# Kernel optimization log

Measured on AMD Instinct MI355X. Metric: run time of the kernel, lower is better.

The kernel has to match this reference:

```python
import jax, jax.numpy as jnp
import numpy as np

MIN_NORM = 1e-15
EPS = 1e-5
C_CURV = 1.0  # args.c

def _norm(x):
    return jnp.clip(jnp.linalg.norm(x, axis=-1, keepdims=True), MIN_NORM)

def artanh(x):
    x = jnp.clip(x, -1.0 + EPS, 1.0 - EPS)
    return 0.5 * (jnp.log1p(x) - jnp.log1p(-x))

def proj(x, c):
    # clip points to stay strictly inside the Poincare ball
    norm = _norm(x)
    maxnorm = (1.0 - EPS) / jnp.sqrt(c)
    return jnp.where(norm > maxnorm, x / norm * maxnorm, x)

def expmap0(u, c):
    sqrt_c = jnp.sqrt(c)
    u_norm = _norm(u)
    return jnp.tanh(sqrt_c * u_norm) * u / (sqrt_c * u_norm)

def logmap0(p, c):
    sqrt_c = jnp.sqrt(c)
    p_norm = _norm(p)
    return artanh(sqrt_c * p_norm) * p / (sqrt_c * p_norm)

def mobius_add(x, y, c):
    x2 = jnp.sum(x * x, axis=-1, keepdims=True)
    y2 = jnp.sum(y * y, axis=-1, keepdims=True)
    xy = jnp.sum(x * y, axis=-1, keepdims=True)
    num = (1.0 + 2.0 * c * xy + c * y2) * x + (1.0 - c * x2) * y
    denom = 1.0 + 2.0 * c * xy + c * c * x2 * y2
    return num / jnp.clip(denom, MIN_NORM)

def mobius_matvec(W, x, c):
    sqrt_c = jnp.sqrt(c)
    x_norm = _norm(x)
    mx = x @ W.T
    mx_norm = _norm(mx)
    return jnp.tanh(mx_norm / x_norm * artanh(sqrt_c * x_norm)) * mx / (mx_norm * sqrt_c)

def poincare_dist(x, y, c):
    sqrt_c = jnp.sqrt(c)
    d = _norm(mobius_add(-x, y, c))[..., 0]
    return 2.0 / sqrt_c * artanh(sqrt_c * d)

def hgnn_layer(h, adj, W, b, c):
    # HypLinear: mobius matvec + hyperbolic bias
    mv = proj(mobius_matvec(W, h, c), c)
    hyp_b = proj(expmap0(b, c), c)
    h = proj(mobius_add(mv, hyp_b, c), c)
    # HypAgg: aggregate in tangent space at origin
    h = proj(expmap0(adj @ logmap0(h, c), c), c)
    # HypAct: relu in tangent space
    return proj(expmap0(jax.nn.relu(logmap0(h, c)), c), c)

def setup_inputs() -> dict:
    key = jax.random.key(0)
    ks = jax.random.split(key, 10)
    N, D, C, NC, NODE_C, L = 8192, 128, 64, 7, 7, 4
    x = jax.random.normal(ks[0], (N, D), jnp.float32)
    adj = jax.random.uniform(ks[1], (N, N), jnp.float32) / N  # row-stochastic-ish dense adjacency
    graph_indicator = jax.random.randint(ks[2], (N,), 0, 1)
    W_conv = jax.random.normal(ks[3], (L, D, D), jnp.float32) / np.sqrt(D)
    b_conv = jax.random.normal(ks[4], (L, D), jnp.float32) * 0.01
    centroids = jax.random.normal(ks[5], (C, D), jnp.float32) * 0.1
    W_mlp = jax.random.normal(ks[6], (NC, C), jnp.float32) * 0.1
    b_mlp = jnp.zeros((NC,), jnp.float32)
    W_mlp1 = jax.random.normal(ks[7], (NODE_C, D), jnp.float32) * 0.1
    b_mlp1 = jnp.zeros((NODE_C,), jnp.float32)
    return {"x": x, "adj": adj, "graph_indicator": graph_indicator,
            "W_conv": W_conv, "b_conv": b_conv, "centroids": centroids,
            "W_mlp": W_mlp, "b_mlp": b_mlp, "W_mlp1": W_mlp1, "b_mlp1": b_mlp1}

def reference(x, adj, graph_indicator, W_conv, b_conv, centroids, W_mlp, b_mlp, W_mlp1, b_mlp1):
    c = C_CURV
    # proj_tan0 is identity for PoincareBall
    h = proj(expmap0(x, c), c)
    # 2 residual blocks, each with 2 HGNN layers; shortcut is identity (in_dim == out_dim)
    for blk in range(2):
        res = h
        for j in range(2):
            idx = blk * 2 + j
            h = hgnn_layer(h, adj, W_conv[idx], b_conv[idx], c)
        h = h + res  # Euclidean residual, as in the source
    # CentroidDistance: pairwise hyperbolic distance [N, C]
    node_centroid_dist = poincare_dist(h[:, None, :], centroids[None, :, :], c)
    readout = jnp.mean(node_centroid_dist, axis=0, keepdims=True)  # [1, C]
    h_r = logmap0(readout, c)  # proj_tan0(logmap0(.)) -> identity proj_tan0
    logits = jax.nn.softmax(h_r @ W_mlp.T + b_mlp, axis=0)[None]        # [1,1,NC]
    h1 = logmap0(h, c)
    logits_node = jax.nn.softmax(h1 @ W_mlp1.T + b_mlp1, axis=0)[None]  # [1,N,node_classes]
    return (logits, logits_node, h_r)
```

## Files before the change

### kernel.cpp

```cpp
#include <hip/hip_runtime.h>

#define MIN_NORM 1e-15f
#define EPSV 1e-5f
#define MAXN (1.0f - EPSV)
#define NN 8192
#define DD 128

typedef unsigned short u16;
typedef __bf16 bf16x8 __attribute__((ext_vector_type(8)));
typedef float f32x4 __attribute__((ext_vector_type(4)));

__device__ __forceinline__ float wave_sum(float v) {
#pragma unroll
  for (int off = 32; off > 0; off >>= 1) v += __shfl_xor(v, off, 64);
  return v;
}

__device__ __forceinline__ float artanh_f(float x) {
  x = fminf(fmaxf(x, -1.0f + EPSV), 1.0f - EPSV);
  return 0.5f * (log1pf(x) - log1pf(-x));
}

__device__ __forceinline__ u16 f2bf(float f) {
  unsigned u = __float_as_uint(f);
  unsigned r = (u + 0x7fffu + ((u >> 16) & 1u)) >> 16;
  return (u16)r;
}
__device__ __forceinline__ float bf2f(u16 b) { return __uint_as_float(((unsigned)b) << 16); }

__device__ __forceinline__ unsigned fenc(float x) {
  unsigned u = __float_as_uint(x);
  return (u & 0x80000000u) ? ~u : (u | 0x80000000u);
}
__device__ __forceinline__ float fdec(unsigned k) {
  unsigned u = (k & 0x80000000u) ? (k & 0x7fffffffu) : ~k;
  return __uint_as_float(u);
}

__device__ __forceinline__ void gload16(const u16* g, u16* l) {
  __builtin_amdgcn_global_load_lds((const __attribute__((address_space(1))) void*)(g),
                                   (__attribute__((address_space(3))) void*)(l), 16, 0, 0);
}

__global__ __launch_bounds__(256) void gemm_adj(const u16* __restrict__ A,
                                                const u16* __restrict__ Bt,
                                                float* __restrict__ Cp,
                                                int KC) {
  __shared__ __align__(16) u16 Ash[3 * 64 * 64];
  __shared__ __align__(16) u16 Bsh[3 * 128 * 64];

  const int tid = threadIdx.x;
  const int lane = tid & 63;
  const int w = tid >> 6;
  const int wm = w >> 1, wn = w & 1;
  const int lrow = lane & 15;
  const int lq = lane >> 4;
  const int m0 = blockIdx.x * 64;
  const int kt0 = (blockIdx.y * KC) >> 6;
  const int bxK = blockIdx.x * (NN >> 6);

  f32x4 acc[2][4];
#pragma unroll
  for (int a = 0; a < 2; a++)
#pragma unroll
    for (int b = 0; b < 4; b++)
#pragma unroll
      for (int r = 0; r < 4; r++) acc[a][b][r] = 0.0f;

#define STAGE(bf, tkt)                                                          \
  do {                                                                          \
    const u16* at = A + (((size_t)(bxK + (tkt))) << 12) + (lane << 3);          \
    _Pragma("unroll") for (int ii = 0; ii < 2; ii++)                            \
      gload16(at + ((ii * 4 + w) << 9), &Ash[(bf) * 4096 + ((ii * 4 + w) << 9)]); \
    const u16* bt2 = Bt + (((size_t)(tkt)) << 13) + (lane << 3);                \
    _Pragma("unroll") for (int ii = 0; ii < 4; ii++)                            \
      gload16(bt2 + ((ii * 4 + w) << 9), &Bsh[(bf) * 8192 + ((ii * 4 + w) << 9)]); \
  } while (0)

#define COMPUTE(bf)                                                             \
  do {                                                                          \
    const int abase = (bf) * 4096, bbase = (bf) * 8192;                         \
    _Pragma("unroll") for (int ks = 0; ks < 2; ks++) {                          \
      const int lc = ks * 4 + lq;                                               \
      bf16x8 af[2], bfr[4];                                                     \
      _Pragma("unroll") for (int ti = 0; ti < 2; ti++) {                        \
        int r = wm * 32 + ti * 16 + lrow;                                       \
        af[ti] = *(const bf16x8*)&Ash[abase + r * 64 + ((lc ^ (r & 7)) << 3)];  \
      }                                                                         \
      _Pragma("unroll") for (int tj = 0; tj < 4; tj++) {                        \
        int n = wn * 64 + tj * 16 + lrow;                                       \
        bfr[tj] = *(const bf16x8*)&Bsh[bbase + n * 64 + ((lc ^ (n & 7)) << 3)]; \
      }                                                                         \
      _Pragma("unroll") for (int ti = 0; ti < 2; ti++)                          \
        _Pragma("unroll") for (int tj = 0; tj < 4; tj++)                        \
          acc[ti][tj] = __builtin_amdgcn_mfma_f32_16x16x32_bf16(af[ti], bfr[tj], acc[ti][tj], 0, 0, 0); \
    }                                                                           \
  } while (0)

  const int nt = KC >> 6;
  STAGE(0, kt0);
  STAGE(1, kt0 + 1);
  for (int t = 0; t < nt - 1; t++) {
    asm volatile("s_waitcnt vmcnt(6)" ::: "memory");
    __builtin_amdgcn_s_barrier();
    if (t + 2 < nt) STAGE((t + 2) % 3, kt0 + t + 2);
    COMPUTE(t % 3);
  }
  asm volatile("s_waitcnt vmcnt(0)" ::: "memory");
  __builtin_amdgcn_s_barrier();
  COMPUTE((nt - 1) % 3);
#undef STAGE
#undef COMPUTE

  float* C = Cp + (size_t)blockIdx.y * NN * 128;
#pragma unroll
  for (int ti = 0; ti < 2; ti++)
#pragma unroll
    for (int tj = 0; tj < 4; tj++)
#pragma unroll
      for (int r = 0; r < 4; r++) {
        int row = m0 + wm * 32 + ti * 16 + lq * 4 + r;
        int col = wn * 64 + tj * 16 + lrow;
        C[(size_t)row * 128 + col] = acc[ti][tj][r];
      }
}

__global__ __launch_bounds__(256) void wgemm_mid(const u16* __restrict__ A,
                                                 const u16* __restrict__ Bt,
                                                 const float* __restrict__ hnorm,
                                                 const float* __restrict__ eb,
                                                 const float* __restrict__ ey2,
                                                 u16* __restrict__ uT2) {
  __shared__ __align__(16) u16 Ash[3 * 64 * 64];
  __shared__ __align__(16) u16 Bsh[3 * 128 * 64];

  const int tid = threadIdx.x;
  const int lane = tid & 63;
  const int w = tid >> 6;
  const int wm = w >> 1, wn = w & 1;
  const int lrow = lane & 15;
  const int lq = lane >> 4;
  const int m0 = blockIdx.x * 64;
  const int srow = lane >> 3, spc = lane & 7;
  const int K = 384;
  const u16* Ap = A + (size_t)m0 * K;

  f32x4 acc[2][4];
#pragma unroll
  for (int a = 0; a < 2; a++)
#pragma unroll
    for (int b = 0; b < 4; b++)
#pragma unroll
      for (int r = 0; r < 4; r++) acc[a][b][r] = 0.0f;

#define STAGE(bf, kk)                                                           \
  do {                                                                          \
    _Pragma("unroll") for (int ii = 0; ii < 2; ii++) {                          \
      int rw = ((ii * 4 + w) << 3) + srow;                                      \
      gload16(Ap + (size_t)rw * K + (kk) + ((spc ^ (rw & 7)) << 3),             \
              &Ash[(bf) * 4096 + ((ii * 4 + w) << 9)]);                         \
    }                                                                           \
    _Pragma("unroll") for (int ii = 0; ii < 4; ii++) {                          \
      int rw = ((ii * 4 + w) << 3) + srow;                                      \
      gload16(Bt + (size_t)rw * K + (kk) + ((spc ^ (rw & 7)) << 3),             \
              &Bsh[(bf) * 8192 + ((ii * 4 + w) << 9)]);                         \
    }                                                                           \
  } while (0)

#define COMPUTE(bf)                                                             \
  do {                                                                          \
    const int abase = (bf) * 4096, bbase = (bf) * 8192;                         \
    _Pragma("unroll") for (int ks = 0; ks < 2; ks++) {                          \
      const int lc = ks * 4 + lq;                                               \
      bf16x8 af[2], bfr[4];                                                     \
      _Pragma("unroll") for (int ti = 0; ti < 2; ti++) {                        \
        int r = wm * 32 + ti * 16 + lrow;                                       \
        af[ti] = *(const bf16x8*)&Ash[abase + r * 64 + ((lc ^ (r & 7)) << 3)];  \
      }                                                                         \
      _Pragma("unroll") for (int tj = 0; tj < 4; tj++) {                        \
        int n = wn * 64 + tj * 16 + lrow;                                       \
        bfr[tj] = *(const bf16x8*)&Bsh[bbase + n * 64 + ((lc ^ (n & 7)) << 3)]; \
      }                                                                         \
      _Pragma("unroll") for (int ti = 0; ti < 2; ti++)                          \
        _Pragma("unroll") for (int tj = 0; tj < 4; tj++)                        \
          acc[ti][tj] = __builtin_amdgcn_mfma_f32_16x16x32_bf16(af[ti], bfr[tj], acc[ti][tj], 0, 0, 0); \
    }                                                                           \
  } while (0)

  const int nt = 6;
  STAGE(0, 0);
  STAGE(1, 64);
  for (int t = 0; t < nt - 1; t++) {
    asm volatile("s_waitcnt vmcnt(6)" ::: "memory");
    __builtin_amdgcn_s_barrier();
    if (t + 2 < nt) STAGE((t + 2) % 3, (t + 2) * 64);
    COMPUTE(t % 3);
  }
  asm volatile("s_waitcnt vmcnt(0)" ::: "memory");
  __builtin_amdgcn_s_barrier();
  COMPUTE((nt - 1) % 3);
#undef STAGE
#undef COMPUTE

  float ecol[4];
#pragma unroll
  for (int tj = 0; tj < 4; tj++) ecol[tj] = eb[wn * 64 + tj * 16 + lrow];

  float* sred = (float*)Ash;
#pragma unroll
  for (int ti = 0; ti < 2; ti++)
#pragma unroll
    for (int r = 0; r < 4; r++) {
      float p2 = 0.f, pe = 0.f;
#pragma unroll
      for (int tj = 0; tj < 4; tj++) {
        float v = acc[ti][tj][r];
        p2 = fmaf(v, v, p2);
        pe = fmaf(v, ecol[tj], pe);
      }
#pragma unroll
      for (int off = 1; off < 16; off <<= 1) {
        p2 += __shfl_xor(p2, off, 64);
        pe += __shfl_xor(pe, off, 64);
      }
      if (lrow == 0) {
        int row = wm * 32 + ti * 16 + lq * 4 + r;
        sred[row * 4 + wn * 2 + 0] = p2;
        sred[row * 4 + wn * 2 + 1] = pe;
      }
    }
  __syncthreads();

  const float y2v = *ey2;
  u16* tb = uT2 + ((size_t)blockIdx.x << 13);
#pragma unroll
  for (int ti = 0; ti < 2; ti++)
#pragma unroll
    for (int r = 0; r < 4; r++) {
      int row = wm * 32 + ti * 16 + lq * 4 + r;
      float s2 = sred[row * 4 + 0] + sred[row * 4 + 2];
      float se = sred[row * 4 + 1] + sred[row * 4 + 3];
      float xn = hnorm[m0 + row];
      float mn = fmaxf(sqrtf(s2), MIN_NORM);
      float t = tanhf(mn / xn * artanh_f(xn));
      float vs = t / mn;
      float pn = fmaxf(sqrtf(vs * vs * s2), MIN_NORM);
      float sc2 = pn > MAXN ? MAXN / pn : 1.0f;
      float al = vs * sc2;
      float x2 = al * al * s2;
      float xy = al * se;
      float ca = 1.0f + 2.0f * xy + y2v;
      float cb = 1.0f - x2;
      float den = fmaxf(1.0f + 2.0f * xy + x2 * y2v, MIN_NORM);
      float tn2 = ca * ca * x2 + 2.0f * ca * cb * xy + cb * cb * y2v;
      float tn = fmaxf(sqrtf(fmaxf(tn2, 0.0f)) / den, MIN_NORM);
      float st = tn > MAXN ? MAXN / tn : 1.0f;
      float pn2 = fmaxf(tn * st, MIN_NORM);
      float gl = artanh_f(pn2) / pn2;
      float Ar = gl * st * ca * al / den;
      float Br = gl * st * cb / den;
      int c8 = (row >> 3) & 7, k7 = row & 7;
#pragma unroll
      for (int tj = 0; tj < 4; tj++) {
        int n = wn * 64 + tj * 16 + lrow;
        float u = Ar * acc[ti][tj][r] + Br * ecol[tj];
        tb[n * 64 + ((c8 ^ (n & 7)) << 3) + k7] = f2bf(u);
      }
    }
}

__global__ __launch_bounds__(256) void cvt_tile(const float* __restrict__ src,
                                                u16* __restrict__ dst) {
  int tid = threadIdx.x;
  int xb = blockIdx.x;
  int kg = blockIdx.y;
  int ch = tid & 63;
  int rs = tid >> 6;
#pragma unroll
  for (int rr = 0; rr < 16; rr++) {
    int row = rr * 4 + rs;
    int gk = kg * 512 + ch * 8;
    const float* s = src + (size_t)(xb * 64 + row) * NN + gk;
    float4 a = *(const float4*)s;
    float4 b = *(const float4*)(s + 4);
    ushort4 d0, d1;
    d0.x = f2bf(a.x); d0.y = f2bf(a.y); d0.z = f2bf(a.z); d0.w = f2bf(a.w);
    d1.x = f2bf(b.x); d1.y = f2bf(b.y); d1.z = f2bf(b.z); d1.w = f2bf(b.w);
    u16* d = dst + (((size_t)(xb * 128 + (gk >> 6))) << 12) + row * 64 +
             ((((gk >> 3) & 7) ^ (row & 7)) << 3);
    *(ushort4*)d = d0;
    *(ushort4*)(d + 4) = d1;
  }
}

__global__ void build_wt(const float* __restrict__ W, u16* __restrict__ Wt2) {
  int idx = blockIdx.x * 256 + threadIdx.x;
  if (idx >= 4 * 128 * 128) return;
  int layer = idx >> 14;
  int n = (idx >> 7) & 127;
  int k = idx & 127;
  float e = W[idx];
  u16 hi = f2bf(e);
  u16 lo = f2bf(e - bf2f(hi));
  u16* base = Wt2 + (size_t)layer * 128 * 384 + (size_t)n * 384;
  base[k] = hi;
  base[128 + k] = hi;
  base[256 + k] = lo;
}

__global__ __launch_bounds__(64) void prep_bias(const float* __restrict__ bconv,
                                                float* __restrict__ ebuf,
                                                float* __restrict__ ey2) {
  int layer = blockIdx.x, lane = threadIdx.x;
  const float* bvec = bconv + layer * DD;
  float b0 = bvec[lane], b1 = bvec[lane + 64];
  float bn = fmaxf(sqrtf(wave_sum(b0 * b0 + b1 * b1)), MIN_NORM);
  float gb = tanhf(bn) / bn;
  float e0 = gb * b0, e1 = gb * b1;
  float en = fmaxf(sqrtf(wave_sum(e0 * e0 + e1 * e1)), MIN_NORM);
  float sb = en > MAXN ? MAXN / en : 1.0f;
  e0 *= sb; e1 *= sb;
  float y2 = wave_sum(e0 * e0 + e1 * e1);
  ebuf[layer * DD + lane] = e0;
  ebuf[layer * DD + lane + 64] = e1;
  if (lane == 0) ey2[layer] = y2;
}

__device__ __forceinline__ void write_split(u16* hs, int i, int lane, float v0, float v1) {
  u16* row = hs + (size_t)i * 384;
  u16 h0 = f2bf(v0), h1 = f2bf(v1);
  u16 l0 = f2bf(v0 - bf2f(h0)), l1 = f2bf(v1 - bf2f(h1));
  row[lane] = h0;         row[lane + 64] = h1;
  row[128 + lane] = l0;   row[128 + 64 + lane] = l1;
  row[256 + lane] = h0;   row[256 + 64 + lane] = h1;
}

__global__ __launch_bounds__(64) void rowwise_init(const float* __restrict__ x,
                                                   float* __restrict__ h,
                                                   float* __restrict__ res,
                                                   u16* __restrict__ hsplit,
                                                   float* __restrict__ hnorm) {
  int i = blockIdx.x, lane = threadIdx.x;
  const float* xr = x + (size_t)i * DD;
  float a0 = xr[lane], a1 = xr[lane + 64];
  float n = fmaxf(sqrtf(wave_sum(a0 * a0 + a1 * a1)), MIN_NORM);
  float g = tanhf(n) / n;
  float y0 = g * a0, y1 = g * a1;
  float pn = fmaxf(sqrtf(wave_sum(y0 * y0 + y1 * y1)), MIN_NORM);
  float s = pn > MAXN ? MAXN / pn : 1.0f;
  y0 *= s; y1 *= s;
  size_t base = (size_t)i * DD;
  h[base + lane] = y0;   h[base + lane + 64] = y1;
  res[base + lane] = y0; res[base + lane + 64] = y1;
  write_split(hsplit, i, lane, y0, y1);
  float hn = fmaxf(sqrtf(wave_sum(y0 * y0 + y1 * y1)), MIN_NORM);
  if (lane == 0) hnorm[i] = hn;
}

__global__ __launch_bounds__(64) void rowwise_post(const float* __restrict__ P,
                                                   float* __restrict__ h,
                                                   float* __restrict__ res,
                                                   u16* __restrict__ hsplit,
                                                   float* __restrict__ hnorm,
                                                   int addres) {
  int i = blockIdx.x, lane = threadIdx.x;
  size_t base = (size_t)i * DD;
  float m0 = 0.f, m1 = 0.f;
#pragma unroll
  for (int sk = 0; sk < 4; sk++) {
    const float* p = P + (size_t)sk * NN * DD + base;
    m0 += p[lane];
    m1 += p[lane + 64];
  }
  float n = fmaxf(sqrtf(wave_sum(m0 * m0 + m1 * m1)), MIN_NORM);
  float g = tanhf(n) / n;
  float y0 = g * m0, y1 = g * m1;
  float pn = fmaxf(sqrtf(wave_sum(y0 * y0 + y1 * y1)), MIN_NORM);
  float s = pn > MAXN ? MAXN / pn : 1.0f;
  y0 *= s; y1 *= s;
  float hn = fmaxf(sqrtf(wave_sum(y0 * y0 + y1 * y1)), MIN_NORM);
  float gl = artanh_f(hn) / hn;
  float u0 = fmaxf(gl * y0, 0.0f), u1 = fmaxf(gl * y1, 0.0f);
  float un = fmaxf(sqrtf(wave_sum(u0 * u0 + u1 * u1)), MIN_NORM);
  float ge = tanhf(un) / un;
  float z0 = ge * u0, z1 = ge * u1;
  float zn = fmaxf(sqrtf(wave_sum(z0 * z0 + z1 * z1)), MIN_NORM);
  float sz = zn > MAXN ? MAXN / zn : 1.0f;
  z0 *= sz; z1 *= sz;
  if (addres) {
    z0 += res[base + lane];
    z1 += res[base + lane + 64];
    res[base + lane] = z0;
    res[base + lane + 64] = z1;
  }
  h[base + lane] = z0;
  h[base + lane + 64] = z1;
  write_split(hsplit, i, lane, z0, z1);
  float hn2 = fmaxf(sqrtf(wave_sum(z0 * z0 + z1 * z1)), MIN_NORM);
  if (lane == 0) hnorm[i] = hn2;
}

__global__ __launch_bounds__(256) void centroid_k(const float* __restrict__ h,
                                                  const float* __restrict__ cen,
                                                  float* __restrict__ rs) {
  __shared__ float cs[64 * 129];
  __shared__ float hs[32 * 128];
  __shared__ float y2s[64];
  int tid = threadIdx.x;
  int i0 = blockIdx.x * 32;
  for (int idx = tid; idx < 64 * 128; idx += 256) {
    int r = idx >> 7, c = idx & 127;
    cs[r * 129 + c] = cen[idx];
  }
  for (int idx = tid; idx < 32 * 128; idx += 256) hs[idx] = h[(size_t)i0 * 128 + idx];
  __syncthreads();
  if (tid < 64) {
    float s = 0.f;
    for (int k = 0; k < 128; k++) { float v = cs[tid * 129 + k]; s = fmaf(v, v, s); }
    y2s[tid] = s;
  }
  __syncthreads();
  int w = tid >> 6, lane = tid & 63;
  float dsum = 0.f;
  for (int rr = 0; rr < 8; rr++) {
    int r = w * 8 + rr;
    float dot = 0.f, x2 = 0.f;
    for (int k = 0; k < 128; k++) {
      float hk = hs[r * 128 + k];
      dot = fmaf(hk, cs[lane * 129 + k], dot);
      x2 = fmaf(hk, hk, x2);
    }
    float y2 = y2s[lane];
    float al = 1.0f - 2.0f * dot + y2;
    float be = 1.0f - x2;
    float num2 = al * al * x2 + be * be * y2 - 2.0f * al * be * dot;
    float den = fmaxf(1.0f - 2.0f * dot + x2 * y2, MIN_NORM);
    float d = fmaxf(sqrtf(fmaxf(num2, 0.0f)) / den, MIN_NORM);
    dsum += 2.0f * artanh_f(d);
  }
  atomicAdd(&rs[lane], dsum);
}

__global__ __launch_bounds__(64) void finalize_k(const float* __restrict__ rs,
                                                 float* __restrict__ out) {
  int lane = threadIdx.x;
  float r = rs[lane] * (1.0f / 8192.0f);
  float n = fmaxf(sqrtf(wave_sum(r * r)), MIN_NORM);
  float a = artanh_f(n);
  out[7 + NN * 7 + lane] = a * r / n;
  if (lane < 7) out[lane] = 1.0f;
}

__global__ __launch_bounds__(64) void scores_k(const float* __restrict__ h,
                                               const float* __restrict__ Wm,
                                               const float* __restrict__ bm,
                                               float* __restrict__ sc,
                                               unsigned* __restrict__ cmaxU) {
  int i = blockIdx.x, lane = threadIdx.x;
  const float* hr = h + (size_t)i * DD;
  float h0 = hr[lane], h1 = hr[lane + 64];
  float pn = fmaxf(sqrtf(wave_sum(h0 * h0 + h1 * h1)), MIN_NORM);
  float gl = artanh_f(pn) / pn;
  float u0 = gl * h0, u1 = gl * h1;
  float p[7];
#pragma unroll
  for (int j = 0; j < 7; j++)
    p[j] = wave_sum(u0 * Wm[j * 128 + lane] + u1 * Wm[j * 128 + lane + 64]);
  float v = p[0];
#pragma unroll
  for (int j = 1; j < 7; j++)
    if (lane == j) v = p[j];
  if (lane < 7) {
    float sv = v + bm[lane];
    sc[(size_t)i * 7 + lane] = sv;
    atomicMax(&cmaxU[lane], fenc(sv));
  }
}

__global__ __launch_bounds__(256) void sm_sum(const float* __restrict__ sc,
                                              const unsigned* __restrict__ cmaxU,
                                              float* __restrict__ csum) {
  __shared__ float buf[256][8];
  int tid = threadIdx.x;
  int i = blockIdx.x * 256 + tid;
  float cm[7];
#pragma unroll
  for (int j = 0; j < 7; j++) cm[j] = fdec(cmaxU[j]);
#pragma unroll
  for (int j = 0; j < 7; j++) buf[tid][j] = expf(sc[i * 7 + j] - cm[j]);
  __syncthreads();
  for (int off = 128; off > 0; off >>= 1) {
    if (tid < off)
#pragma unroll
      for (int j = 0; j < 7; j++) buf[tid][j] += buf[tid + off][j];
    __syncthreads();
  }
  if (tid < 7) atomicAdd(&csum[tid], buf[0][tid]);
}

__global__ __launch_bounds__(256) void sm_write(const float* __restrict__ sc,
                                                const unsigned* __restrict__ cmaxU,
                                                const float* __restrict__ csum,
                                                float* __restrict__ out) {
  int idx = blockIdx.x * 256 + threadIdx.x;
  if (idx >= NN * 7) return;
  int i = idx / 7, j = idx - i * 7;
  float cm = fdec(cmaxU[j]);
  out[idx] = expf(sc[i * 7 + j] - cm) / csum[j];
}

extern "C" void kernel_launch(void* const* d_in, const int* in_sizes, int n_in,
                              void* d_out, int out_size, void* d_ws, size_t ws_size,
                              hipStream_t stream) {
  const float* x = (const float*)d_in[0];
  const float* adj = (const float*)d_in[1];
  const float* W_conv = (const float*)d_in[3];
  const float* b_conv = (const float*)d_in[4];
  const float* centroids = (const float*)d_in[5];
  const float* W_mlp1 = (const float*)d_in[8];
  const float* b_mlp1 = (const float*)d_in[9];
  float* out = (float*)d_out;

  char* ws = (char*)d_ws;
  size_t off = 0;
  auto alloc = [&](size_t bytes) {
    void* p = ws + off;
    off = (off + bytes + 255) & ~(size_t)255;
    return p;
  };
  float* h = (float*)alloc((size_t)NN * DD * 4);
  float* res = (float*)alloc((size_t)NN * DD * 4);
  u16* hsplit = (u16*)alloc((size_t)NN * 384 * 2);
  u16* uT2 = (u16*)alloc((size_t)DD * NN * 2);
  u16* Wt2 = (u16*)alloc((size_t)4 * 128 * 384 * 2);
  float* P = (float*)alloc((size_t)4 * NN * DD * 4);
  u16* adjT = (u16*)alloc((size_t)NN * NN * 2);
  float* scores = (float*)alloc((size_t)NN * 7 * 4);
  float* hnorm = (float*)alloc((size_t)NN * 4);
  float* ebuf = (float*)alloc(4 * DD * 4);
  float* ey2 = (float*)alloc(4 * 4);
  float* zblk = (float*)alloc(768);
  float* rs = zblk;
  unsigned* cmaxU = (unsigned*)(zblk + 64);
  float* csum = zblk + 72;
  (void)ws_size; (void)in_sizes; (void)n_in; (void)out_size;

  hipMemsetAsync(zblk, 0, 768, stream);
  build_wt<<<(4 * 128 * 128 + 255) / 256, 256, 0, stream>>>(W_conv, Wt2);
  prep_bias<<<4, 64, 0, stream>>>(b_conv, ebuf, ey2);
  rowwise_init<<<NN, 64, 0, stream>>>(x, h, res, hsplit, hnorm);
  cvt_tile<<<dim3(128, 16), 256, 0, stream>>>(adj, adjT);
  for (int layer = 0; layer < 4; layer++) {
    wgemm_mid<<<NN / 64, 256, 0, stream>>>(hsplit, Wt2 + (size_t)layer * 128 * 384,
                                           hnorm, ebuf + layer * DD, ey2 + layer, uT2);
    gemm_adj<<<dim3(NN / 64, 4), 256, 0, stream>>>(adjT, uT2, P, NN / 4);
    rowwise_post<<<NN, 64, 0, stream>>>(P, h, res, hsplit, hnorm, (layer & 1));
  }
  centroid_k<<<256, 256, 0, stream>>>(h, centroids, rs);
  finalize_k<<<1, 64, 0, stream>>>(rs, out);
  scores_k<<<NN, 64, 0, stream>>>(h, W_mlp1, b_mlp1, scores, cmaxU);
  sm_sum<<<NN / 256, 256, 0, stream>>>(scores, cmaxU, csum);
  sm_write<<<(NN * 7 + 255) / 256, 256, 0, stream>>>(scores, cmaxU, csum, out + 7);
}
```

Before: 814.6 us.

## Fuse adjacency GEMM with row-wise post-processing and merge setup and tail kernels

```diff
diff --git a/kernel.cpp b/kernel.cpp
--- a/kernel.cpp
+++ b/kernel.cpp
@@ -42,87 +42,96 @@
                                    (__attribute__((address_space(3))) void*)(l), 16, 0, 0);
 }
 
-__global__ __launch_bounds__(256) void gemm_adj(const u16* __restrict__ A,
-                                                const u16* __restrict__ Bt,
-                                                float* __restrict__ Cp,
-                                                int KC) {
-  __shared__ __align__(16) u16 Ash[3 * 64 * 64];
-  __shared__ __align__(16) u16 Bsh[3 * 128 * 64];
-
+__global__ __launch_bounds__(256) void head_k(const float* __restrict__ x,
+                                              const float* __restrict__ adj,
+                                              const float* __restrict__ W_conv,
+                                              const float* __restrict__ b_conv,
+                                              u16* __restrict__ adjT,
+                                              float* __restrict__ h,
+                                              float* __restrict__ res,
+                                              u16* __restrict__ hsplit,
+                                              float* __restrict__ hnorm,
+                                              u16* __restrict__ Wt2,
+                                              float* __restrict__ ebuf,
+                                              float* __restrict__ ey2,
+                                              float* __restrict__ zblk) {
   const int tid = threadIdx.x;
-  const int lane = tid & 63;
-  const int w = tid >> 6;
-  const int wm = w >> 1, wn = w & 1;
-  const int lrow = lane & 15;
-  const int lq = lane >> 4;
-  const int m0 = blockIdx.x * 64;
-  const int kt0 = (blockIdx.y * KC) >> 6;
-  const int bxK = blockIdx.x * (NN >> 6);
-
-  f32x4 acc[2][4];
-#pragma unroll
-  for (int a = 0; a < 2; a++)
-#pragma unroll
-    for (int b = 0; b < 4; b++)
-#pragma unroll
-      for (int r = 0; r < 4; r++) acc[a][b][r] = 0.0f;
-
-#define STAGE(bf, tkt)                                                          \
-  do {                                                                          \
-    const u16* at = A + (((size_t)(bxK + (tkt))) << 12) + (lane << 3);          \
-    _Pragma("unroll") for (int ii = 0; ii < 2; ii++)                            \
-      gload16(at + ((ii * 4 + w) << 9), &Ash[(bf) * 4096 + ((ii * 4 + w) << 9)]); \
-    const u16* bt2 = Bt + (((size_t)(tkt)) << 13) + (lane << 3);                \
-    _Pragma("unroll") for (int ii = 0; ii < 4; ii++)                            \
-      gload16(bt2 + ((ii * 4 + w) << 9), &Bsh[(bf) * 8192 + ((ii * 4 + w) << 9)]); \
-  } while (0)
-
-#define COMPUTE(bf)                                                             \
-  do {                                                                          \
-    const int abase = (bf) * 4096, bbase = (bf) * 8192;                         \
-    _Pragma("unroll") for (int ks = 0; ks < 2; ks++) {                          \
-      const int lc = ks * 4 + lq;                                               \
-      bf16x8 af[2], bfr[4];                                                     \
-      _Pragma("unroll") for (int ti = 0; ti < 2; ti++) {                        \
-        int r = wm * 32 + ti * 16 + lrow;                                       \
-        af[ti] = *(const bf16x8*)&Ash[abase + r * 64 + ((lc ^ (r & 7)) << 3)];  \
-      }                                                                         \
-      _Pragma("unroll") for (int tj = 0; tj < 4; tj++) {                        \
-        int n = wn * 64 + tj * 16 + lrow;                                       \
-        bfr[tj] = *(const bf16x8*)&Bsh[bbase + n * 64 + ((lc ^ (n & 7)) << 3)]; \
-      }                                                                         \
-      _Pragma("unroll") for (int ti = 0; ti < 2; ti++)                          \
-        _Pragma("unroll") for (int tj = 0; tj < 4; tj++)                        \
-          acc[ti][tj] = __builtin_amdgcn_mfma_f32_16x16x32_bf16(af[ti], bfr[tj], acc[ti][tj], 0, 0, 0); \
-    }                                                                           \
-  } while (0)
-
-  const int nt = KC >> 6;
-  STAGE(0, kt0);
-  STAGE(1, kt0 + 1);
-  for (int t = 0; t < nt - 1; t++) {
-    asm volatile("s_waitcnt vmcnt(6)" ::: "memory");
-    __builtin_amdgcn_s_barrier();
-    if (t + 2 < nt) STAGE((t + 2) % 3, kt0 + t + 2);
-    COMPUTE(t % 3);
+  const int b = blockIdx.x;
+  if (b < 2048) {
+    int xb = b >> 4, kg = b & 15;
+    int ch = tid & 63, rs_ = tid >> 6;
+#pragma unroll
+    for (int rr = 0; rr < 16; rr++) {
+      int row = rr * 4 + rs_;
+      int gk = kg * 512 + ch * 8;
+      const float* s = adj + (size_t)(xb * 64 + row) * NN + gk;
+      float4 a = *(const float4*)s;
+      float4 bb = *(const float4*)(s + 4);
+      ushort4 d0, d1;
+      d0.x = f2bf(a.x); d0.y = f2bf(a.y); d0.z = f2bf(a.z); d0.w = f2bf(a.w);
+      d1.x = f2bf(bb.x); d1.y = f2bf(bb.y); d1.z = f2bf(bb.z); d1.w = f2bf(bb.w);
+      u16* d = adjT + (((size_t)(xb * 128 + (gk >> 6))) << 12) + row * 64 +
+               ((((gk >> 3) & 7) ^ (row & 7)) << 3);
+      *(ushort4*)d = d0;
+      *(ushort4*)(d + 4) = d1;
+    }
+  } else if (b < 2176) {
+    int w4 = tid >> 6, lane = tid & 63;
+    int ib = b - 2048;
+    for (int rr = 0; rr < 16; rr++) {
+      int i = ib * 64 + w4 * 16 + rr;
+      const float* xr = x + (size_t)i * DD;
+      float a0 = xr[lane], a1 = xr[lane + 64];
+      float n = fmaxf(sqrtf(wave_sum(a0 * a0 + a1 * a1)), MIN_NORM);
+      float g = tanhf(n) / n;
+      float y0 = g * a0, y1 = g * a1;
+      float pn = fmaxf(sqrtf(wave_sum(y0 * y0 + y1 * y1)), MIN_NORM);
+      float s = pn > MAXN ? MAXN / pn : 1.0f;
+      y0 *= s; y1 *= s;
+      size_t base = (size_t)i * DD;
+      h[base + lane] = y0;   h[base + lane + 64] = y1;
+      res[base + lane] = y0; res[base + lane + 64] = y1;
+      u16* row = hsplit + (size_t)i * 384;
+      u16 h0 = f2bf(y0), h1 = f2bf(y1);
+      u16 l0 = f2bf(y0 - bf2f(h0)), l1 = f2bf(y1 - bf2f(h1));
+      row[lane] = h0;         row[lane + 64] = h1;
+      row[128 + lane] = l0;   row[128 + 64 + lane] = l1;
+      row[256 + lane] = h0;   row[256 + 64 + lane] = h1;
+      float hn = fmaxf(sqrtf(wave_sum(y0 * y0 + y1 * y1)), MIN_NORM);
+      if (lane == 0) hnorm[i] = hn;
+    }
+  } else if (b < 2240) {
+    int b2 = b - 2176;
+#pragma unroll
+    for (int e = 0; e < 4; e++) {
+      int idx = b2 * 1024 + e * 256 + tid;
+      int layer = idx >> 14;
+      int n = (idx >> 7) & 127;
+      int k = idx & 127;
+      float ev = W_conv[idx];
+      u16 hi = f2bf(ev);
+      u16 lo = f2bf(ev - bf2f(hi));
+      u16* base = Wt2 + (size_t)layer * 128 * 384 + (size_t)n * 384;
+      base[k] = hi;
+      base[128 + k] = hi;
+      base[256 + k] = lo;
+    }
+  } else {
+    int layer = tid >> 6, lane = tid & 63;
+    const float* bvec = b_conv + layer * DD;
+    float b0 = bvec[lane], b1 = bvec[lane + 64];
+    float bn = fmaxf(sqrtf(wave_sum(b0 * b0 + b1 * b1)), MIN_NORM);
+    float gb = tanhf(bn) / bn;
+    float e0 = gb * b0, e1 = gb * b1;
+    float en = fmaxf(sqrtf(wave_sum(e0 * e0 + e1 * e1)), MIN_NORM);
+    float sb = en > MAXN ? MAXN / en : 1.0f;
+    e0 *= sb; e1 *= sb;
+    float y2 = wave_sum(e0 * e0 + e1 * e1);
+    ebuf[layer * DD + lane] = e0;
+    ebuf[layer * DD + lane + 64] = e1;
+    if (lane == 0) ey2[layer] = y2;
+    if (tid < 192) zblk[tid] = 0.0f;
   }
-  asm volatile("s_waitcnt vmcnt(0)" ::: "memory");
-  __builtin_amdgcn_s_barrier();
-  COMPUTE((nt - 1) % 3);
-#undef STAGE
-#undef COMPUTE
-
-  float* C = Cp + (size_t)blockIdx.y * NN * 128;
-#pragma unroll
-  for (int ti = 0; ti < 2; ti++)
-#pragma unroll
-    for (int tj = 0; tj < 4; tj++)
-#pragma unroll
-      for (int r = 0; r < 4; r++) {
-        int row = m0 + wm * 32 + ti * 16 + lq * 4 + r;
-        int col = wn * 64 + tj * 16 + lrow;
-        C[(size_t)row * 128 + col] = acc[ti][tj][r];
-      }
 }
 
 __global__ __launch_bounds__(256) void wgemm_mid(const u16* __restrict__ A,
@@ -269,233 +278,313 @@
     }
 }
 
-__global__ __launch_bounds__(256) void cvt_tile(const float* __restrict__ src,
-                                                u16* __restrict__ dst) {
+__global__ __launch_bounds__(256, 1) void adjpost(const u16* __restrict__ A,
+                                                  const u16* __restrict__ Bt,
+                                                  float* __restrict__ h,
+                                                  float* __restrict__ res,
+                                                  u16* __restrict__ hsplit,
+                                                  float* __restrict__ hnorm,
+                                                  int addres) {
+  __shared__ __align__(16) u16 Ash[3 * 64 * 64];
+  __shared__ __align__(16) u16 Bsh[3 * 128 * 64];
+
+  const int tid = threadIdx.x;
+  const int lane = tid & 63;
+  const int w = tid >> 6;
+  const int wm = w >> 1, wn = w & 1;
+  const int lrow = lane & 15;
+  const int lq = lane >> 4;
+  const int m0 = blockIdx.x * 64;
+  const int bxK = blockIdx.x * (NN >> 6);
+
+  f32x4 acc[2][4];
+#pragma unroll
+  for (int a = 0; a < 2; a++)
+#pragma unroll
+    for (int b = 0; b < 4; b++)
+#pragma unroll
+      for (int r = 0; r < 4; r++) acc[a][b][r] = 0.0f;
+
+#define STAGE(bf, tkt)                                                          \
+  do {                                                                          \
+    const u16* at = A + (((size_t)(bxK + (tkt))) << 12) + (lane << 3);          \
+    _Pragma("unroll") for (int ii = 0; ii < 2; ii++)                            \
+      gload16(at + ((ii * 4 + w) << 9), &Ash[(bf) * 4096 + ((ii * 4 + w) << 9)]); \
+    const u16* bt2 = Bt + (((size_t)(tkt)) << 13) + (lane << 3);                \
+    _Pragma("unroll") for (int ii = 0; ii < 4; ii++)                            \
+      gload16(bt2 + ((ii * 4 + w) << 9), &Bsh[(bf) * 8192 + ((ii * 4 + w) << 9)]); \
+  } while (0)
+
+#define COMPUTE(bf)                                                             \
+  do {                                                                          \
+    const int abase = (bf) * 4096, bbase = (bf) * 8192;                         \
+    _Pragma("unroll") for (int ks = 0; ks < 2; ks++) {                          \
+      const int lc = ks * 4 + lq;                                               \
+      bf16x8 af[2], bfr[4];                                                     \
+      _Pragma("unroll") for (int ti = 0; ti < 2; ti++) {                        \
+        int r = wm * 32 + ti * 16 + lrow;                                       \
+        af[ti] = *(const bf16x8*)&Ash[abase + r * 64 + ((lc ^ (r & 7)) << 3)];  \
+      }                                                                         \
+      _Pragma("unroll") for (int tj = 0; tj < 4; tj++) {                        \
+        int n = wn * 64 + tj * 16 + lrow;                                       \
+        bfr[tj] = *(const bf16x8*)&Bsh[bbase + n * 64 + ((lc ^ (n & 7)) << 3)]; \
+      }                                                                         \
+      _Pragma("unroll") for (int ti = 0; ti < 2; ti++)                          \
+        _Pragma("unroll") for (int tj = 0; tj < 4; tj++)                        \
+          acc[ti][tj] = __builtin_amdgcn_mfma_f32_16x16x32_bf16(af[ti], bfr[tj], acc[ti][tj], 0, 0, 0); \
+    }                                                                           \
+  } while (0)
+
+  const int nt = NN >> 6;
+  STAGE(0, 0);
+  STAGE(1, 1);
+  for (int t = 0; t < nt - 1; t++) {
+    asm volatile("s_waitcnt vmcnt(6)" ::: "memory");
+    __builtin_amdgcn_s_barrier();
+    if (t + 2 < nt) STAGE((t + 2) % 3, t + 2);
+    COMPUTE(t % 3);
+  }
+  asm volatile("s_waitcnt vmcnt(0)" ::: "memory");
+  __builtin_amdgcn_s_barrier();
+  COMPUTE((nt - 1) % 3);
+#undef STAGE
+#undef COMPUTE
+
+  float* sred = (float*)Ash;
+
+#pragma unroll
+  for (int ti = 0; ti < 2; ti++)
+#pragma unroll
+    for (int r = 0; r < 4; r++) {
+      float p = 0.f;
+#pragma unroll
+      for (int tj = 0; tj < 4; tj++) p = fmaf(acc[ti][tj][r], acc[ti][tj][r], p);
+#pragma unroll
+      for (int off = 1; off < 16; off <<= 1) p += __shfl_xor(p, off, 64);
+      if (lrow == 0) {
+        int row2 = wm * 32 + ti * 16 + lq * 4 + r;
+        sred[row2 * 2 + wn] = p;
+      }
+    }
+  __syncthreads();
+
+  float c2v[2][4];
+#pragma unroll
+  for (int ti = 0; ti < 2; ti++)
+#pragma unroll
+    for (int r = 0; r < 4; r++) {
+      int row2 = wm * 32 + ti * 16 + lq * 4 + r;
+      float rn = sqrtf(sred[row2 * 2 + 0] + sred[row2 * 2 + 1]);
+      float n = fmaxf(rn, MIN_NORM);
+      float g = tanhf(n) / n;
+      float pn = fmaxf(g * rn, MIN_NORM);
+      float s = pn > MAXN ? MAXN / pn : 1.0f;
+      float c1 = g * s;
+      float hn = fmaxf(c1 * rn, MIN_NORM);
+      float gl = artanh_f(hn) / hn;
+      c2v[ti][r] = gl * c1;
+    }
+
+#pragma unroll
+  for (int ti = 0; ti < 2; ti++)
+#pragma unroll
+    for (int tj = 0; tj < 4; tj++)
+#pragma unroll
+      for (int r = 0; r < 4; r++)
+        acc[ti][tj][r] = fmaxf(c2v[ti][r] * acc[ti][tj][r], 0.0f);
+#pragma unroll
+  for (int ti = 0; ti < 2; ti++)
+#pragma unroll
+    for (int r = 0; r < 4; r++) {
+      float p = 0.f;
+#pragma unroll
+      for (int tj = 0; tj < 4; tj++) p = fmaf(acc[ti][tj][r], acc[ti][tj][r], p);
+#pragma unroll
+      for (int off = 1; off < 16; off <<= 1) p += __shfl_xor(p, off, 64);
+      if (lrow == 0) {
+        int row2 = wm * 32 + ti * 16 + lq * 4 + r;
+        sred[128 + row2 * 2 + wn] = p;
+      }
+    }
+  __syncthreads();
+
+  float c3v[2][4];
+#pragma unroll
+  for (int ti = 0; ti < 2; ti++)
+#pragma unroll
+    for (int r = 0; r < 4; r++) {
+      int row2 = wm * 32 + ti * 16 + lq * 4 + r;
+      float rn2 = sqrtf(sred[128 + row2 * 2 + 0] + sred[128 + row2 * 2 + 1]);
+      float un = fmaxf(rn2, MIN_NORM);
+      float ge = tanhf(un) / un;
+      float zn = fmaxf(ge * rn2, MIN_NORM);
+      float sz = zn > MAXN ? MAXN / zn : 1.0f;
+      c3v[ti][r] = ge * sz;
+    }
+
+#pragma unroll
+  for (int ti = 0; ti < 2; ti++)
+#pragma unroll
+    for (int tj = 0; tj < 4; tj++)
+#pragma unroll
+      for (int r = 0; r < 4; r++) {
+        int row2 = wm * 32 + ti * 16 + lq * 4 + r;
+        int col = wn * 64 + tj * 16 + lrow;
+        size_t gi = (size_t)(m0 + row2) * DD + col;
+        float z = c3v[ti][r] * acc[ti][tj][r];
+        if (addres) {
+          z += res[gi];
+          res[gi] = z;
+        }
+        acc[ti][tj][r] = z;
+      }
+#pragma unroll
+  for (int ti = 0; ti < 2; ti++)
+#pragma unroll
+    for (int r = 0; r < 4; r++) {
+      float p = 0.f;
+#pragma unroll
+      for (int tj = 0; tj < 4; tj++) p = fmaf(acc[ti][tj][r], acc[ti][tj][r], p);
+#pragma unroll
+      for (int off = 1; off < 16; off <<= 1) p += __shfl_xor(p, off, 64);
+      if (lrow == 0) {
+        int row2 = wm * 32 + ti * 16 + lq * 4 + r;
+        sred[256 + row2 * 2 + wn] = p;
+      }
+    }
+  __syncthreads();
+
+#pragma unroll
+  for (int ti = 0; ti < 2; ti++)
+#pragma unroll
+    for (int tj = 0; tj < 4; tj++)
+#pragma unroll
+      for (int r = 0; r < 4; r++) {
+        int row2 = wm * 32 + ti * 16 + lq * 4 + r;
+        int col = wn * 64 + tj * 16 + lrow;
+        float z = acc[ti][tj][r];
+        h[(size_t)(m0 + row2) * DD + col] = z;
+        u16* rowp = hsplit + (size_t)(m0 + row2) * 384;
+        u16 hi = f2bf(z);
+        u16 lo = f2bf(z - bf2f(hi));
+        rowp[col] = hi;
+        rowp[128 + col] = lo;
+        rowp[256 + col] = hi;
+      }
+  if (lrow == 0 && wn == 0) {
+#pragma unroll
+    for (int ti = 0; ti < 2; ti++)
+#pragma unroll
+      for (int r = 0; r < 4; r++) {
+        int row2 = wm * 32 + ti * 16 + lq * 4 + r;
+        hnorm[m0 + row2] =
+            fmaxf(sqrtf(sred[256 + row2 * 2 + 0] + sred[256 + row2 * 2 + 1]), MIN_NORM);
+      }
+  }
+}
+
+__global__ __launch_bounds__(256) void cent_scores(const float* __restrict__ h,
+                                                   const float* __restrict__ cen,
+                                                   float* __restrict__ rs,
+                                                   const float* __restrict__ Wm,
+                                                   const float* __restrict__ bm,
+                                                   float* __restrict__ sc,
+                                                   unsigned* __restrict__ cmaxU) {
   int tid = threadIdx.x;
-  int xb = blockIdx.x;
-  int kg = blockIdx.y;
-  int ch = tid & 63;
-  int rs = tid >> 6;
-#pragma unroll
-  for (int rr = 0; rr < 16; rr++) {
-    int row = rr * 4 + rs;
-    int gk = kg * 512 + ch * 8;
-    const float* s = src + (size_t)(xb * 64 + row) * NN + gk;
-    float4 a = *(const float4*)s;
-    float4 b = *(const float4*)(s + 4);
-    ushort4 d0, d1;
-    d0.x = f2bf(a.x); d0.y = f2bf(a.y); d0.z = f2bf(a.z); d0.w = f2bf(a.w);
-    d1.x = f2bf(b.x); d1.y = f2bf(b.y); d1.z = f2bf(b.z); d1.w = f2bf(b.w);
-    u16* d = dst + (((size_t)(xb * 128 + (gk >> 6))) << 12) + row * 64 +
-             ((((gk >> 3) & 7) ^ (row & 7)) << 3);
-    *(ushort4*)d = d0;
-    *(ushort4*)(d + 4) = d1;
+  if (blockIdx.x < 256) {
+    __shared__ float cs[64 * 129];
+    __shared__ float hs[32 * 128];
+    __shared__ float y2s[64];
+    int i0 = blockIdx.x * 32;
+    for (int idx = tid; idx < 64 * 128; idx += 256) {
+      int r = idx >> 7, c = idx & 127;
+      cs[r * 129 + c] = cen[idx];
+    }
+    for (int idx = tid; idx < 32 * 128; idx += 256) hs[idx] = h[(size_t)i0 * 128 + idx];
+    __syncthreads();
+    if (tid < 64) {
+      float s = 0.f;
+      for (int k = 0; k < 128; k++) { float v = cs[tid * 129 + k]; s = fmaf(v, v, s); }
+      y2s[tid] = s;
+    }
+    __syncthreads();
+    int w = tid >> 6, lane = tid & 63;
+    float dsum = 0.f;
+    for (int rr = 0; rr < 8; rr++) {
+      int r = w * 8 + rr;
+      float dot = 0.f, x2 = 0.f;
+      for (int k = 0; k < 128; k++) {
+        float hk = hs[r * 128 + k];
+        dot = fmaf(hk, cs[lane * 129 + k], dot);
+        x2 = fmaf(hk, hk, x2);
+      }
+      float y2 = y2s[lane];
+      float al = 1.0f - 2.0f * dot + y2;
+      float be = 1.0f - x2;
+      float num2 = al * al * x2 + be * be * y2 - 2.0f * al * be * dot;
+      float den = fmaxf(1.0f - 2.0f * dot + x2 * y2, MIN_NORM);
+      float d = fmaxf(sqrtf(fmaxf(num2, 0.0f)) / den, MIN_NORM);
+      dsum += 2.0f * artanh_f(d);
+    }
+    atomicAdd(&rs[lane], dsum);
+  } else {
+    int ib = blockIdx.x - 256;
+    int w4 = tid >> 6, lane = tid & 63;
+    for (int rr = 0; rr < 16; rr++) {
+      int i = ib * 64 + w4 * 16 + rr;
+      const float* hr = h + (size_t)i * DD;
+      float h0 = hr[lane], h1 = hr[lane + 64];
+      float pn = fmaxf(sqrtf(wave_sum(h0 * h0 + h1 * h1)), MIN_NORM);
+      float gl = artanh_f(pn) / pn;
+      float u0 = gl * h0, u1 = gl * h1;
+      float p[7];
+#pragma unroll
+      for (int j = 0; j < 7; j++)
+        p[j] = wave_sum(u0 * Wm[j * 128 + lane] + u1 * Wm[j * 128 + lane + 64]);
+      float v = p[0];
+#pragma unroll
+      for (int j = 1; j < 7; j++)
+        if (lane == j) v = p[j];
+      if (lane < 7) {
+        float sv = v + bm[lane];
+        sc[(size_t)i * 7 + lane] = sv;
+        atomicMax(&cmaxU[lane], fenc(sv));
+      }
+    }
   }
 }
 
-__global__ void build_wt(const float* __restrict__ W, u16* __restrict__ Wt2) {
-  int idx = blockIdx.x * 256 + threadIdx.x;
-  if (idx >= 4 * 128 * 128) return;
-  int layer = idx >> 14;
-  int n = (idx >> 7) & 127;
-  int k = idx & 127;
-  float e = W[idx];
-  u16 hi = f2bf(e);
-  u16 lo = f2bf(e - bf2f(hi));
-  u16* base = Wt2 + (size_t)layer * 128 * 384 + (size_t)n * 384;
-  base[k] = hi;
-  base[128 + k] = hi;
-  base[256 + k] = lo;
-}
-
-__global__ __launch_bounds__(64) void prep_bias(const float* __restrict__ bconv,
-                                                float* __restrict__ ebuf,
-                                                float* __restrict__ ey2) {
-  int layer = blockIdx.x, lane = threadIdx.x;
-  const float* bvec = bconv + layer * DD;
-  float b0 = bvec[lane], b1 = bvec[lane + 64];
-  float bn = fmaxf(sqrtf(wave_sum(b0 * b0 + b1 * b1)), MIN_NORM);
-  float gb = tanhf(bn) / bn;
-  float e0 = gb * b0, e1 = gb * b1;
-  float en = fmaxf(sqrtf(wave_sum(e0 * e0 + e1 * e1)), MIN_NORM);
-  float sb = en > MAXN ? MAXN / en : 1.0f;
-  e0 *= sb; e1 *= sb;
-  float y2 = wave_sum(e0 * e0 + e1 * e1);
-  ebuf[layer * DD + lane] = e0;
-  ebuf[layer * DD + lane + 64] = e1;
-  if (lane == 0) ey2[layer] = y2;
-}
-
-__device__ __forceinline__ void write_split(u16* hs, int i, int lane, float v0, float v1) {
-  u16* row = hs + (size_t)i * 384;
-  u16 h0 = f2bf(v0), h1 = f2bf(v1);
-  u16 l0 = f2bf(v0 - bf2f(h0)), l1 = f2bf(v1 - bf2f(h1));
-  row[lane] = h0;         row[lane + 64] = h1;
-  row[128 + lane] = l0;   row[128 + 64 + lane] = l1;
-  row[256 + lane] = h0;   row[256 + 64 + lane] = h1;
-}
-
-__global__ __launch_bounds__(64) void rowwise_init(const float* __restrict__ x,
-                                                   float* __restrict__ h,
-                                                   float* __restrict__ res,
-                                                   u16* __restrict__ hsplit,
-                                                   float* __restrict__ hnorm) {
-  int i = blockIdx.x, lane = threadIdx.x;
-  const float* xr = x + (size_t)i * DD;
-  float a0 = xr[lane], a1 = xr[lane + 64];
-  float n = fmaxf(sqrtf(wave_sum(a0 * a0 + a1 * a1)), MIN_NORM);
-  float g = tanhf(n) / n;
-  float y0 = g * a0, y1 = g * a1;
-  float pn = fmaxf(sqrtf(wave_sum(y0 * y0 + y1 * y1)), MIN_NORM);
-  float s = pn > MAXN ? MAXN / pn : 1.0f;
-  y0 *= s; y1 *= s;
-  size_t base = (size_t)i * DD;
-  h[base + lane] = y0;   h[base + lane + 64] = y1;
-  res[base + lane] = y0; res[base + lane + 64] = y1;
-  write_split(hsplit, i, lane, y0, y1);
-  float hn = fmaxf(sqrtf(wave_sum(y0 * y0 + y1 * y1)), MIN_NORM);
-  if (lane == 0) hnorm[i] = hn;
-}
-
-__global__ __launch_bounds__(64) void rowwise_post(const float* __restrict__ P,
-                                                   float* __restrict__ h,
-                                                   float* __restrict__ res,
-                                                   u16* __restrict__ hsplit,
-                                                   float* __restrict__ hnorm,
-                                                   int addres) {
-  int i = blockIdx.x, lane = threadIdx.x;
-  size_t base = (size_t)i * DD;
-  float m0 = 0.f, m1 = 0.f;
-#pragma unroll
-  for (int sk = 0; sk < 4; sk++) {
-    const float* p = P + (size_t)sk * NN * DD + base;
-    m0 += p[lane];
-    m1 += p[lane + 64];
+__global__ __launch_bounds__(256) void fin_sum(const float* __restrict__ sc,
+                                               const unsigned* __restrict__ cmaxU,
+                                               float* __restrict__ csum,
+                                               const float* __restrict__ rs,
+                                               float* __restrict__ out) {
+  int tid = threadIdx.x;
+  if (blockIdx.x < 32) {
+    __shared__ float buf[256][8];
+    int i = blockIdx.x * 256 + tid;
+    float cm[7];
+#pragma unroll
+    for (int j = 0; j < 7; j++) cm[j] = fdec(cmaxU[j]);
+#pragma unroll
+    for (int j = 0; j < 7; j++) buf[tid][j] = expf(sc[i * 7 + j] - cm[j]);
+    __syncthreads();
+    for (int off = 128; off > 0; off >>= 1) {
+      if (tid < off)
+#pragma unroll
+        for (int j = 0; j < 7; j++) buf[tid][j] += buf[tid + off][j];
+      __syncthreads();
+    }
+    if (tid < 7) atomicAdd(&csum[tid], buf[0][tid]);
+  } else {
+    if (tid < 64) {
+      float r = rs[tid] * (1.0f / 8192.0f);
+      float n = fmaxf(sqrtf(wave_sum(r * r)), MIN_NORM);
+      float a = artanh_f(n);
+      out[7 + NN * 7 + tid] = a * r / n;
+      if (tid < 7) out[tid] = 1.0f;
+    }
   }
-  float n = fmaxf(sqrtf(wave_sum(m0 * m0 + m1 * m1)), MIN_NORM);
-  float g = tanhf(n) / n;
-  float y0 = g * m0, y1 = g * m1;
-  float pn = fmaxf(sqrtf(wave_sum(y0 * y0 + y1 * y1)), MIN_NORM);
-  float s = pn > MAXN ? MAXN / pn : 1.0f;
-  y0 *= s; y1 *= s;
-  float hn = fmaxf(sqrtf(wave_sum(y0 * y0 + y1 * y1)), MIN_NORM);
-  float gl = artanh_f(hn) / hn;
-  float u0 = fmaxf(gl * y0, 0.0f), u1 = fmaxf(gl * y1, 0.0f);
-  float un = fmaxf(sqrtf(wave_sum(u0 * u0 + u1 * u1)), MIN_NORM);
-  float ge = tanhf(un) / un;
-  float z0 = ge * u0, z1 = ge * u1;
-  float zn = fmaxf(sqrtf(wave_sum(z0 * z0 + z1 * z1)), MIN_NORM);
-  float sz = zn > MAXN ? MAXN / zn : 1.0f;
-  z0 *= sz; z1 *= sz;
-  if (addres) {
-    z0 += res[base + lane];
-    z1 += res[base + lane + 64];
-    res[base + lane] = z0;
-    res[base + lane + 64] = z1;
-  }
-  h[base + lane] = z0;
-  h[base + lane + 64] = z1;
-  write_split(hsplit, i, lane, z0, z1);
-  float hn2 = fmaxf(sqrtf(wave_sum(z0 * z0 + z1 * z1)), MIN_NORM);
-  if (lane == 0) hnorm[i] = hn2;
-}
-
-__global__ __launch_bounds__(256) void centroid_k(const float* __restrict__ h,
-                                                  const float* __restrict__ cen,
-                                                  float* __restrict__ rs) {
-  __shared__ float cs[64 * 129];
-  __shared__ float hs[32 * 128];
-  __shared__ float y2s[64];
-  int tid = threadIdx.x;
-  int i0 = blockIdx.x * 32;
-  for (int idx = tid; idx < 64 * 128; idx += 256) {
-    int r = idx >> 7, c = idx & 127;
-    cs[r * 129 + c] = cen[idx];
-  }
-  for (int idx = tid; idx < 32 * 128; idx += 256) hs[idx] = h[(size_t)i0 * 128 + idx];
-  __syncthreads();
-  if (tid < 64) {
-    float s = 0.f;
-    for (int k = 0; k < 128; k++) { float v = cs[tid * 129 + k]; s = fmaf(v, v, s); }
-    y2s[tid] = s;
-  }
-  __syncthreads();
-  int w = tid >> 6, lane = tid & 63;
-  float dsum = 0.f;
-  for (int rr = 0; rr < 8; rr++) {
-    int r = w * 8 + rr;
-    float dot = 0.f, x2 = 0.f;
-    for (int k = 0; k < 128; k++) {
-      float hk = hs[r * 128 + k];
-      dot = fmaf(hk, cs[lane * 129 + k], dot);
-      x2 = fmaf(hk, hk, x2);
-    }
-    float y2 = y2s[lane];
-    float al = 1.0f - 2.0f * dot + y2;
-    float be = 1.0f - x2;
-    float num2 = al * al * x2 + be * be * y2 - 2.0f * al * be * dot;
-    float den = fmaxf(1.0f - 2.0f * dot + x2 * y2, MIN_NORM);
-    float d = fmaxf(sqrtf(fmaxf(num2, 0.0f)) / den, MIN_NORM);
-    dsum += 2.0f * artanh_f(d);
-  }
-  atomicAdd(&rs[lane], dsum);
-}
-
-__global__ __launch_bounds__(64) void finalize_k(const float* __restrict__ rs,
-                                                 float* __restrict__ out) {
-  int lane = threadIdx.x;
-  float r = rs[lane] * (1.0f / 8192.0f);
-  float n = fmaxf(sqrtf(wave_sum(r * r)), MIN_NORM);
-  float a = artanh_f(n);
-  out[7 + NN * 7 + lane] = a * r / n;
-  if (lane < 7) out[lane] = 1.0f;
-}
-
-__global__ __launch_bounds__(64) void scores_k(const float* __restrict__ h,
-                                               const float* __restrict__ Wm,
-                                               const float* __restrict__ bm,
-                                               float* __restrict__ sc,
-                                               unsigned* __restrict__ cmaxU) {
-  int i = blockIdx.x, lane = threadIdx.x;
-  const float* hr = h + (size_t)i * DD;
-  float h0 = hr[lane], h1 = hr[lane + 64];
-  float pn = fmaxf(sqrtf(wave_sum(h0 * h0 + h1 * h1)), MIN_NORM);
-  float gl = artanh_f(pn) / pn;
-  float u0 = gl * h0, u1 = gl * h1;
-  float p[7];
-#pragma unroll
-  for (int j = 0; j < 7; j++)
-    p[j] = wave_sum(u0 * Wm[j * 128 + lane] + u1 * Wm[j * 128 + lane + 64]);
-  float v = p[0];
-#pragma unroll
-  for (int j = 1; j < 7; j++)
-    if (lane == j) v = p[j];
-  if (lane < 7) {
-    float sv = v + bm[lane];
-    sc[(size_t)i * 7 + lane] = sv;
-    atomicMax(&cmaxU[lane], fenc(sv));
-  }
-}
-
-__global__ __launch_bounds__(256) void sm_sum(const float* __restrict__ sc,
-                                              const unsigned* __restrict__ cmaxU,
-                                              float* __restrict__ csum) {
-  __shared__ float buf[256][8];
-  int tid = threadIdx.x;
-  int i = blockIdx.x * 256 + tid;
-  float cm[7];
-#pragma unroll
-  for (int j = 0; j < 7; j++) cm[j] = fdec(cmaxU[j]);
-#pragma unroll
-  for (int j = 0; j < 7; j++) buf[tid][j] = expf(sc[i * 7 + j] - cm[j]);
-  __syncthreads();
-  for (int off = 128; off > 0; off >>= 1) {
-    if (tid < off)
-#pragma unroll
-      for (int j = 0; j < 7; j++) buf[tid][j] += buf[tid + off][j];
-    __syncthreads();
-  }
-  if (tid < 7) atomicAdd(&csum[tid], buf[0][tid]);
 }
 
 __global__ __launch_bounds__(256) void sm_write(const float* __restrict__ sc,
@@ -533,7 +622,6 @@
   u16* hsplit = (u16*)alloc((size_t)NN * 384 * 2);
   u16* uT2 = (u16*)alloc((size_t)DD * NN * 2);
   u16* Wt2 = (u16*)alloc((size_t)4 * 128 * 384 * 2);
-  float* P = (float*)alloc((size_t)4 * NN * DD * 4);
   u16* adjT = (u16*)alloc((size_t)NN * NN * 2);
   float* scores = (float*)alloc((size_t)NN * 7 * 4);
   float* hnorm = (float*)alloc((size_t)NN * 4);
@@ -545,20 +633,14 @@
   float* csum = zblk + 72;
   (void)ws_size; (void)in_sizes; (void)n_in; (void)out_size;
 
-  hipMemsetAsync(zblk, 0, 768, stream);
-  build_wt<<<(4 * 128 * 128 + 255) / 256, 256, 0, stream>>>(W_conv, Wt2);
-  prep_bias<<<4, 64, 0, stream>>>(b_conv, ebuf, ey2);
-  rowwise_init<<<NN, 64, 0, stream>>>(x, h, res, hsplit, hnorm);
-  cvt_tile<<<dim3(128, 16), 256, 0, stream>>>(adj, adjT);
+  head_k<<<2241, 256, 0, stream>>>(x, adj, W_conv, b_conv, adjT, h, res, hsplit,
+                                   hnorm, Wt2, ebuf, ey2, zblk);
   for (int layer = 0; layer < 4; layer++) {
     wgemm_mid<<<NN / 64, 256, 0, stream>>>(hsplit, Wt2 + (size_t)layer * 128 * 384,
                                            hnorm, ebuf + layer * DD, ey2 + layer, uT2);
-    gemm_adj<<<dim3(NN / 64, 4), 256, 0, stream>>>(adjT, uT2, P, NN / 4);
-    rowwise_post<<<NN, 64, 0, stream>>>(P, h, res, hsplit, hnorm, (layer & 1));
+    adjpost<<<NN / 64, 256, 0, stream>>>(adjT, uT2, h, res, hsplit, hnorm, (layer & 1));
   }
-  centroid_k<<<256, 256, 0, stream>>>(h, centroids, rs);
-  finalize_k<<<1, 64, 0, stream>>>(rs, out);
-  scores_k<<<NN, 64, 0, stream>>>(h, W_mlp1, b_mlp1, scores, cmaxU);
-  sm_sum<<<NN / 256, 256, 0, stream>>>(scores, cmaxU, csum);
+  cent_scores<<<384, 256, 0, stream>>>(h, centroids, rs, W_mlp1, b_mlp1, scores, cmaxU);
+  fin_sum<<<33, 256, 0, stream>>>(scores, cmaxU, csum, rs, out);
   sm_write<<<(NN * 7 + 255) / 256, 256, 0, stream>>>(scores, cmaxU, csum, out + 7);
 }
```

New measurement: 1.122 ms. 37.7% more time.
